# Optimization experiments

Hardware: AMD Instinct MI355X
Metric: run time of the kernel (lower is better)

## Reference

```python
import jax, jax.numpy as jnp
import numpy as np

LEVELS = 16
BASE_RES = 16.0
MAX_RES = 2048.0
MAX_PARAMS = 2 ** 19
FEAT = 2
LOG_B = np.log(MAX_RES / BASE_RES) / (LEVELS - 1)
PRIMES = np.array([1, 2654435761, 805459861], dtype=np.uint32)


def level_meta():
    # Replays HashEncoder.__init__ offset/size bookkeeping.
    offsets, sizes, ress = [], [], []
    offset = 0
    begin_fast = LEVELS
    for i in range(LEVELS):
        res = int(np.ceil(BASE_RES * np.exp(i * LOG_B) - 1.0) + 1)  # grid_resolution
        full = float(res) ** 3
        aligned = int((full + 7) / 8) * 8  # align_to(full, 8)
        size = int(min(MAX_PARAMS, aligned))
        if full > size and begin_fast == LEVELS:
            begin_fast = i
        offsets.append(offset)
        sizes.append(size)
        ress.append(res)
        offset += size
    return offsets, sizes, ress, begin_fast, offset


OFFSETS, SIZES, RESS, BEGIN_FAST, TOTAL = level_meta()


def setup_inputs():
    key = jax.random.key(0)
    k1, k2 = jax.random.split(key)
    B = 2_000_000
    positions = jax.random.uniform(k1, (B, 3), dtype=jnp.float32)  # xyz in [0,1)
    table = jax.random.uniform(k2, (TOTAL, FEAT), dtype=jnp.float32,
                               minval=-1e-4, maxval=1e-4)
    return {"positions": positions, "table": table}


def _encode(positions, table):
    outs = []
    for level in range(LEVELS):  # fixed small structural loop (16 levels)
        scale = np.float32(BASE_RES * np.exp(level * LOG_B) - 1.0)  # grid_scale
        res = RESS[level]
        pos = positions * scale + 0.5          # [B,3]
        grid_f = jnp.floor(pos)
        frac = pos - grid_f                    # [B,3] trilinear fractions
        grid = grid_f.astype(jnp.uint32)
        acc = jnp.zeros((positions.shape[0], FEAT), dtype=jnp.float32)
        for corner in range(8):                # 8 cube corners (static unroll)
            sel = np.array([(corner >> d) & 1 for d in range(3)], dtype=np.uint32)
            pg = grid + sel                    # [B,3] uint32 corner coords
            w = jnp.prod(jnp.where(sel.astype(bool), frac, 1.0 - frac), axis=-1)  # [B]
            if level < BEGIN_FAST:
                # dense 'under_hash': x + y*res + z*res^2 (uint32 wraparound ok)
                strides = np.array([1, res, res * res], dtype=np.uint32)
                h = jnp.sum(pg * strides, axis=-1, dtype=jnp.uint32)
            else:
                # spatial 'fast_hash': xor of coord*prime with uint32 wraparound
                h = (pg[:, 0] * PRIMES[0]) ^ (pg[:, 1] * PRIMES[1]) ^ (pg[:, 2] * PRIMES[2])
            idx = (h % np.uint32(SIZES[level])).astype(jnp.int32) + OFFSETS[level]
            acc = acc + w[:, None] * table[idx]  # irregular gather [B,FEAT]
        outs.append(acc)
    # matches output_embedding[i, level].view(-1, levels*feat): level-major, feat inner
    return jnp.concatenate(outs, axis=-1)  # [B, LEVELS*FEAT]


def reference(positions, table):
    return _encode(positions, table)
```

## Files before the change

kernel.cpp:

```cpp
#include <hip/hip_runtime.h>
#include <math.h>

#define NLEVELS 16
#define BEGIN_FAST 5
#define P2 2654435761u
#define P3 805459861u
#define FAST_MASK 524287u
#define DENSE_TOTAL 330952u

constexpr unsigned kRes[NLEVELS] = {16u, 23u, 31u, 43u, 59u, 81u, 112u, 154u, 213u, 295u, 407u, 562u, 777u, 1073u, 1483u, 2048u};
constexpr unsigned kSize[NLEVELS] = {
    4096u, 12168u, 29792u, 79512u, 205384u,
    524288u, 524288u, 524288u, 524288u, 524288u, 524288u,
    524288u, 524288u, 524288u, 524288u, 524288u};
constexpr unsigned kOffset[NLEVELS] = {
    0u,       4096u,    16264u,   46056u,   125568u,  330952u,
    855240u,  1379528u, 1903816u, 2428104u, 2952392u, 3476680u,
    4000968u, 4525256u, 5049544u, 5573832u};

struct Scales {
    float s[NLEVELS];
};

typedef float fvec2 __attribute__((ext_vector_type(2)));
typedef float fvec4 __attribute__((ext_vector_type(4)));
typedef unsigned uvec2 __attribute__((ext_vector_type(2)));

__device__ __forceinline__ unsigned bfpack(float a, float b) {
    unsigned ua = __float_as_uint(a);
    unsigned ub = __float_as_uint(b);
    ua = (ua + 0x7FFFu + ((ua >> 16) & 1u)) >> 16;
    ub = (ub + 0x7FFFu + ((ub >> 16) & 1u)) & 0xFFFF0000u;
    return ua | ub;
}
__device__ __forceinline__ float bf_lo(unsigned e) { return __uint_as_float(e << 16); }
__device__ __forceinline__ float bf_hi(unsigned e) { return __uint_as_float(e & 0xFFFF0000u); }

__global__ __launch_bounds__(256) void convert_dense_kernel(
    const float2* __restrict__ table,
    uvec2* __restrict__ E,
    int total)
{
    int j = blockIdx.x * 256 + threadIdx.x;
    if (j >= total) return;
    int l = 0;
    if (j >= (int)kOffset[1]) l = 1;
    if (j >= (int)kOffset[2]) l = 2;
    if (j >= (int)kOffset[3]) l = 3;
    if (j >= (int)kOffset[4]) l = 4;
    const unsigned jl = (unsigned)j - kOffset[l];
    const unsigned jn = (jl + 1u == kSize[l]) ? 0u : jl + 1u;
    const float2 t0 = table[kOffset[l] + jl];
    const float2 t1 = table[kOffset[l] + jn];
    uvec2 r = {bfpack(t0.x, t0.y), bfpack(t1.x, t1.y)};
    __builtin_nontemporal_store(r, E + j);
}

__global__ __launch_bounds__(256) void fine_level_kernel(
    const float* __restrict__ positions,
    const float2* __restrict__ tab,
    float2* __restrict__ wsl,
    int B, float s)
{
    int p = blockIdx.x * 256 + threadIdx.x;
    if (p >= B) return;

    const float x = __builtin_nontemporal_load(positions + 3 * p + 0);
    const float y = __builtin_nontemporal_load(positions + 3 * p + 1);
    const float z = __builtin_nontemporal_load(positions + 3 * p + 2);

    const float px = x * s + 0.5f;
    const float py = y * s + 0.5f;
    const float pz = z * s + 0.5f;
    const float flx = floorf(px), fly = floorf(py), flz = floorf(pz);
    const float rx = px - flx, ry = py - fly, rz = pz - flz;
    const unsigned gx = (unsigned)flx;
    const unsigned gy = (unsigned)fly;
    const unsigned gz = (unsigned)flz;
    const float wx0 = 1.0f - rx, wy0 = 1.0f - ry, wz0 = 1.0f - rz;

    const unsigned hy0 = gy * P2, hy1 = hy0 + P2;
    const unsigned hz0 = gz * P3, hz1 = hz0 + P3;

    float ax = 0.0f, ay = 0.0f;
#pragma unroll
    for (int c = 0; c < 8; ++c) {
        const unsigned cx = (unsigned)(c & 1);
        const unsigned cy = (unsigned)((c >> 1) & 1);
        const unsigned cz = (unsigned)((c >> 2) & 1);
        const float w = (cx ? rx : wx0) * (cy ? ry : wy0) * (cz ? rz : wz0);
        const unsigned h = (gx + cx) ^ (cy ? hy1 : hy0) ^ (cz ? hz1 : hz0);
        const float2 t = tab[h & FAST_MASK];
        ax += w * t.x;
        ay += w * t.y;
    }
    fvec2 r = {ax, ay};
    __builtin_nontemporal_store(r, reinterpret_cast<fvec2*>(wsl) + p);
}

__global__ __launch_bounds__(256) void dense_kernel(
    const float* __restrict__ positions,
    const uvec2* __restrict__ E,
    unsigned* __restrict__ dws,
    int B, Scales sc)
{
    int p = blockIdx.x * 256 + threadIdx.x;
    if (p >= B) return;

    const float x = __builtin_nontemporal_load(positions + 3 * p + 0);
    const float y = __builtin_nontemporal_load(positions + 3 * p + 1);
    const float z = __builtin_nontemporal_load(positions + 3 * p + 2);

#pragma unroll
    for (int l = 0; l < BEGIN_FAST; ++l) {
        const float s = sc.s[l];
        const float px = x * s + 0.5f;
        const float py = y * s + 0.5f;
        const float pz = z * s + 0.5f;
        const float flx = floorf(px), fly = floorf(py), flz = floorf(pz);
        const float rx = px - flx, ry = py - fly, rz = pz - flz;
        const unsigned gx = (unsigned)flx;
        const unsigned gy = (unsigned)fly;
        const unsigned gz = (unsigned)flz;
        const float wx0 = 1.0f - rx, wy0 = 1.0f - ry, wz0 = 1.0f - rz;

        const uvec2* tab = E + kOffset[l];
        const unsigned res = kRes[l];

        float ax = 0.0f, ay = 0.0f;
#pragma unroll
        for (int cc = 0; cc < 4; ++cc) {
            const unsigned cy = (unsigned)(cc & 1);
            const unsigned cz = (unsigned)(cc >> 1);
            const float wyz = (cy ? ry : wy0) * (cz ? rz : wz0);
            const unsigned h0 = gx + (gy + cy) * res + (gz + cz) * (res * res);
            const unsigned idx0 = h0 % kSize[l];
            const uvec2 q = tab[idx0];
            ax += wyz * (wx0 * bf_lo(q.x) + rx * bf_lo(q.y));
            ay += wyz * (wx0 * bf_hi(q.x) + rx * bf_hi(q.y));
        }
        __builtin_nontemporal_store(bfpack(ax, ay), dws + (size_t)l * (size_t)B + p);
    }
}

__global__ __launch_bounds__(256) void merge_kernel(
    const unsigned* __restrict__ dws,
    const float2* __restrict__ fws,
    float* __restrict__ out,
    int B)
{
    int p = blockIdx.x * 256 + threadIdx.x;
    if (p >= B) return;

    float o[2 * NLEVELS];
#pragma unroll
    for (int l = 0; l < BEGIN_FAST; ++l) {
        const unsigned v = __builtin_nontemporal_load(dws + (size_t)l * (size_t)B + p);
        o[2 * l + 0] = bf_lo(v);
        o[2 * l + 1] = bf_hi(v);
    }
#pragma unroll
    for (int l = BEGIN_FAST; l < NLEVELS; ++l) {
        const fvec2 v = __builtin_nontemporal_load(
            reinterpret_cast<const fvec2*>(fws) + (size_t)(l - BEGIN_FAST) * (size_t)B + p);
        o[2 * l + 0] = v.x;
        o[2 * l + 1] = v.y;
    }
    float* op = out + (size_t)p * (2 * NLEVELS);
#pragma unroll
    for (int i = 0; i < 8; ++i) {
        fvec4 v = {o[4 * i + 0], o[4 * i + 1], o[4 * i + 2], o[4 * i + 3]};
        *(reinterpret_cast<fvec4*>(op) + i) = v;
    }
}

__global__ __launch_bounds__(256) void hash_encode_kernel(
    const float* __restrict__ positions,
    const float2* __restrict__ table,
    float* __restrict__ out,
    int B, Scales sc)
{
    int p = blockIdx.x * 256 + threadIdx.x;
    if (p >= B) return;

    const float x = positions[3 * p + 0];
    const float y = positions[3 * p + 1];
    const float z = positions[3 * p + 2];

    float o[2 * NLEVELS];

#pragma unroll
    for (int l = 0; l < NLEVELS; ++l) {
        const float s = sc.s[l];
        const float px = x * s + 0.5f;
        const float py = y * s + 0.5f;
        const float pz = z * s + 0.5f;
        const float flx = floorf(px), fly = floorf(py), flz = floorf(pz);
        const float rx = px - flx, ry = py - fly, rz = pz - flz;
        const unsigned gx = (unsigned)flx;
        const unsigned gy = (unsigned)fly;
        const unsigned gz = (unsigned)flz;
        const float wx0 = 1.0f - rx, wy0 = 1.0f - ry, wz0 = 1.0f - rz;

        float ax = 0.0f, ay = 0.0f;
#pragma unroll
        for (int c = 0; c < 8; ++c) {
            const unsigned cx = (unsigned)(c & 1);
            const unsigned cy = (unsigned)((c >> 1) & 1);
            const unsigned cz = (unsigned)((c >> 2) & 1);
            const unsigned pgx = gx + cx;
            const unsigned pgy = gy + cy;
            const unsigned pgz = gz + cz;
            const float w = (cx ? rx : wx0) * (cy ? ry : wy0) * (cz ? rz : wz0);
            unsigned h;
            if (l < BEGIN_FAST) {
                h = pgx + pgy * kRes[l] + pgz * (kRes[l] * kRes[l]);
            } else {
                h = pgx ^ (pgy * P2) ^ (pgz * P3);
            }
            const unsigned idx = (h % kSize[l]) + kOffset[l];
            const float2 t = table[idx];
            ax += w * t.x;
            ay += w * t.y;
        }
        o[2 * l + 0] = ax;
        o[2 * l + 1] = ay;
    }

    float* op = out + (size_t)p * (2 * NLEVELS);
#pragma unroll
    for (int i = 0; i < 8; ++i) {
        fvec4 v = {o[4 * i + 0], o[4 * i + 1], o[4 * i + 2], o[4 * i + 3]};
        *(reinterpret_cast<fvec4*>(op) + i) = v;
    }
}

extern "C" void kernel_launch(void* const* d_in, const int* in_sizes, int n_in,
                              void* d_out, int out_size, void* d_ws, size_t ws_size,
                              hipStream_t stream) {
    const float* positions = (const float*)d_in[0];
    const float2* table = (const float2*)d_in[1];
    float* out = (float*)d_out;

    const int B = in_sizes[0] / 3;

    Scales sc;
    const double log_b = log(2048.0 / 16.0) / (NLEVELS - 1);
    for (int l = 0; l < NLEVELS; ++l) {
        sc.s[l] = (float)(16.0 * exp((double)l * log_b) - 1.0);
    }

    const int blocks = (B + 255) / 256;

    const size_t dws_bytes = 5u * (size_t)B * sizeof(unsigned);
    const size_t fws_bytes = 11u * (size_t)B * sizeof(float2);
    const size_t E_bytes = (size_t)DENSE_TOTAL * sizeof(uvec2);
    const size_t ws_need = dws_bytes + fws_bytes + E_bytes;

    if (ws_size >= ws_need) {
        unsigned* dws = (unsigned*)d_ws;
        float2* fws = (float2*)((char*)d_ws + dws_bytes);
        uvec2* E = (uvec2*)((char*)d_ws + dws_bytes + fws_bytes);

        convert_dense_kernel<<<((int)DENSE_TOTAL + 255) / 256, 256, 0, stream>>>(
            table, E, (int)DENSE_TOTAL);

        for (int l = BEGIN_FAST; l < NLEVELS; ++l) {
            fine_level_kernel<<<blocks, 256, 0, stream>>>(
                positions, table + kOffset[l],
                fws + (size_t)(l - BEGIN_FAST) * (size_t)B, B, sc.s[l]);
        }
        dense_kernel<<<blocks, 256, 0, stream>>>(positions, E, dws, B, sc);
        merge_kernel<<<blocks, 256, 0, stream>>>(dws, fws, out, B);
    } else {
        hash_encode_kernel<<<blocks, 256, 0, stream>>>(positions, table, out, B, sc);
    }
}
```

Measured before the change: 817.5 us.

## Fuse dense-level encoding into merge kernel and stage level-0 table in LDS

Merges the dense-level kernel with the merge kernel, so the dense results stay in registers instead of passing through a bf16-packed workspace, which removes one write and one read pass over 5*B words and one launch. Each block also copies the 4096-entry level-0 packed table into shared memory and gathers level 0 from it. In exchange, every block pays a 32KB LDS fill and a barrier, and the larger LDS use may lower occupancy. Dense outputs also skip the bf16 repack, so they differ slightly from before.

```diff
diff --git a/kernel.cpp b/kernel.cpp
--- a/kernel.cpp
+++ b/kernel.cpp
@@ -98,18 +98,27 @@
     __builtin_nontemporal_store(r, reinterpret_cast<fvec2*>(wsl) + p);
 }
 
-__global__ __launch_bounds__(256) void dense_kernel(
+__global__ __launch_bounds__(256) void dense_merge_kernel(
     const float* __restrict__ positions,
     const uvec2* __restrict__ E,
-    unsigned* __restrict__ dws,
+    const float2* __restrict__ fws,
+    float* __restrict__ out,
     int B, Scales sc)
 {
-    int p = blockIdx.x * 256 + threadIdx.x;
+    __shared__ uvec2 lds_E0[4096];
+    for (int i = threadIdx.x; i < 4096; i += 256) {
+        lds_E0[i] = E[i];
+    }
+    __syncthreads();
+
+    const int p = blockIdx.x * 256 + threadIdx.x;
     if (p >= B) return;
 
     const float x = __builtin_nontemporal_load(positions + 3 * p + 0);
     const float y = __builtin_nontemporal_load(positions + 3 * p + 1);
     const float z = __builtin_nontemporal_load(positions + 3 * p + 2);
+
+    float o[2 * NLEVELS];
 
 #pragma unroll
     for (int l = 0; l < BEGIN_FAST; ++l) {
@@ -135,30 +144,14 @@
             const float wyz = (cy ? ry : wy0) * (cz ? rz : wz0);
             const unsigned h0 = gx + (gy + cy) * res + (gz + cz) * (res * res);
             const unsigned idx0 = h0 % kSize[l];
-            const uvec2 q = tab[idx0];
+            const uvec2 q = (l == 0) ? lds_E0[idx0] : tab[idx0];
             ax += wyz * (wx0 * bf_lo(q.x) + rx * bf_lo(q.y));
             ay += wyz * (wx0 * bf_hi(q.x) + rx * bf_hi(q.y));
         }
-        __builtin_nontemporal_store(bfpack(ax, ay), dws + (size_t)l * (size_t)B + p);
-    }
-}
-
-__global__ __launch_bounds__(256) void merge_kernel(
-    const unsigned* __restrict__ dws,
-    const float2* __restrict__ fws,
-    float* __restrict__ out,
-    int B)
-{
-    int p = blockIdx.x * 256 + threadIdx.x;
-    if (p >= B) return;
-
-    float o[2 * NLEVELS];
-#pragma unroll
-    for (int l = 0; l < BEGIN_FAST; ++l) {
-        const unsigned v = __builtin_nontemporal_load(dws + (size_t)l * (size_t)B + p);
-        o[2 * l + 0] = bf_lo(v);
-        o[2 * l + 1] = bf_hi(v);
-    }
+        o[2 * l + 0] = ax;
+        o[2 * l + 1] = ay;
+    }
+
 #pragma unroll
     for (int l = BEGIN_FAST; l < NLEVELS; ++l) {
         const fvec2 v = __builtin_nontemporal_load(
@@ -166,6 +159,7 @@
         o[2 * l + 0] = v.x;
         o[2 * l + 1] = v.y;
     }
+
     float* op = out + (size_t)p * (2 * NLEVELS);
 #pragma unroll
     for (int i = 0; i < 8; ++i) {
@@ -252,15 +246,13 @@
 
     const int blocks = (B + 255) / 256;
 
-    const size_t dws_bytes = 5u * (size_t)B * sizeof(unsigned);
     const size_t fws_bytes = 11u * (size_t)B * sizeof(float2);
     const size_t E_bytes = (size_t)DENSE_TOTAL * sizeof(uvec2);
-    const size_t ws_need = dws_bytes + fws_bytes + E_bytes;
+    const size_t ws_need = fws_bytes + E_bytes;
 
     if (ws_size >= ws_need) {
-        unsigned* dws = (unsigned*)d_ws;
-        float2* fws = (float2*)((char*)d_ws + dws_bytes);
-        uvec2* E = (uvec2*)((char*)d_ws + dws_bytes + fws_bytes);
+        float2* fws = (float2*)d_ws;
+        uvec2* E = (uvec2*)((char*)d_ws + fws_bytes);
 
         convert_dense_kernel<<<((int)DENSE_TOTAL + 255) / 256, 256, 0, stream>>>(
             table, E, (int)DENSE_TOTAL);
@@ -270,8 +262,7 @@
                 positions, table + kOffset[l],
                 fws + (size_t)(l - BEGIN_FAST) * (size_t)B, B, sc.s[l]);
         }
-        dense_kernel<<<blocks, 256, 0, stream>>>(positions, E, dws, B, sc);
-        merge_kernel<<<blocks, 256, 0, stream>>>(dws, fws, out, B);
+        dense_merge_kernel<<<blocks, 256, 0, stream>>>(positions, E, fws, out, B, sc);
     } else {
         hash_encode_kernel<<<blocks, 256, 0, stream>>>(positions, table, out, B, sc);
     }
```

New measurement: 812.1 us. No clear change (-0.7%).
